# Performance work log

Measured on AMD Instinct MI355X. Metric: run time of the kernel, lower is better.

The kernel has to match this reference:

```python
import jax, jax.numpy as jnp
import numpy as np

B, N, H, D, FE = 4, 1024, 64, 64, 16  # batch, nodes, hidden_in, out_dim, edge_feat


def setup_inputs() -> dict:
    key = jax.random.key(0)
    k0, k1, k2, k3 = jax.random.split(key, 4)
    h0 = jax.random.normal(k0, (B, N, H), dtype=jnp.float32)
    e = jax.random.normal(k1, (B, N, N, FE), dtype=jnp.float32)
    # fc: Linear(H -> D, bias=False), xavier-normal-ish scale
    w_fc = jax.random.normal(k2, (D, H), dtype=jnp.float32) * (2.0 / np.sqrt(H + D))
    # attn_fc: Linear(2*D + FE -> 1, bias=False), stored as a flat vector
    w_attn = jax.random.normal(k3, (2 * D + FE,), dtype=jnp.float32) * (2.0 / np.sqrt(2 * D + FE + 1))
    return {"h0": h0, "e": e, "w_fc": w_fc, "w_attn": w_attn}


def reference(h0, e, w_fc, w_attn):
    # z = fc(h0): [B, N, D]
    z = jnp.einsum('bnh,dh->bnd', h0, w_fc)
    d = z.shape[-1]
    # attn_fc on concat(z1, z2, m): z1[i*N+j] = z[j], z2[i*N+j] = z[i], m[i*N+j] = e[i, j]
    a1, a2, a3 = w_attn[:d], w_attn[d:2 * d], w_attn[2 * d:]
    sj = jnp.einsum('bnd,d->bn', z, a1)            # score part from z1 (source j)
    si = jnp.einsum('bnd,d->bn', z, a2)            # score part from z2 (target i)
    se = jnp.einsum('bijf,f->bij', e, a3)          # edge score part
    # scores s[b, i, j], then leaky_relu (slope 0.01 as in torch default)
    s = jax.nn.leaky_relu(si[:, :, None] + sj[:, None, :] + se)
    # softmax over the flattened N*N pair axis (dim=1 of [B, N*N, 1] in torch)
    b = s.shape[0]
    alpha = jax.nn.softmax(s.reshape(b, -1), axis=1).reshape(s.shape)  # [B, N, N]
    # h_t[b, i] = sum_j alpha[b, i, j] * z_expanded[b, i, j], where z_expanded[b, i, j] = z[b, i]
    h_t = jnp.sum(alpha, axis=2)[:, :, None] * z
    return h_t
```

## Files before the change

kernel.cpp:

```cpp
#include <hip/hip_runtime.h>
#include <hip/hip_bf16.h>

#define NTOK   1024
#define NROWS  4096
#define HD     64

__global__ __launch_bounds__(256) void k1_fc(
    const float* __restrict__ h0, const float* __restrict__ w_fc,
    const float* __restrict__ w_attn,
    float* __restrict__ z, float* __restrict__ si, float* __restrict__ sj)
{
    __shared__ float wfs[HD * 65];
    __shared__ float h0s[16 * HD];

    const int tid = threadIdx.x;
    for (int k = tid; k < HD * HD; k += 256) {
        int d = k >> 6, h = k & 63;
        wfs[d * 65 + h] = w_fc[k];
    }
    const int row0 = blockIdx.x * 16;
    for (int k = tid; k < 16 * HD; k += 256)
        h0s[k] = h0[row0 * HD + k];
    __syncthreads();

    const int lane = tid & 63, wave = tid >> 6;
    const float a1 = w_attn[lane];
    const float a2 = w_attn[HD + lane];

    for (int rr = wave; rr < 16; rr += 4) {
        float acc = 0.f;
        #pragma unroll
        for (int h = 0; h < HD; ++h)
            acc = fmaf(h0s[rr * HD + h], wfs[lane * 65 + h], acc);
        const int row = row0 + rr;
        z[row * HD + lane] = acc;

        float v1 = acc * a1, v2 = acc * a2;
        #pragma unroll
        for (int off = 32; off; off >>= 1) {
            v1 += __shfl_xor(v1, off);
            v2 += __shfl_xor(v2, off);
        }
        if (lane == 0) { sj[row] = v1; si[row] = v2; }
    }
}

__global__ __launch_bounds__(256) void k2_row(
    const float* __restrict__ e, const float* __restrict__ w_attn,
    const float* __restrict__ si, const float* __restrict__ sj,
    float* __restrict__ Mrow, float* __restrict__ Rrow)
{
    const int row = blockIdx.x;
    const int b   = row >> 10;
    const int tid = threadIdx.x;

    const float4* a3v = (const float4*)(w_attn + 2 * HD);
    const float4  a3q = a3v[tid & 3];

    const float   si_r = si[row];
    const float4* ev   = (const float4*)(e + (size_t)row * (NTOK * 16));
    const float*  sjb  = sj + b * NTOK;

    float sv[16];
    #pragma unroll
    for (int it = 0; it < 16; ++it) {
        const int c = it * 256 + tid;
        const float4 ec = ev[c];
        float p = ec.x * a3q.x + ec.y * a3q.y + ec.z * a3q.z + ec.w * a3q.w;
        p += __shfl_xor(p, 1);
        p += __shfl_xor(p, 2);
        const int j = it * 64 + (tid >> 2);
        float s = si_r + sjb[j] + p;
        s = (s > 0.f) ? s : 0.01f * s;
        sv[it] = s;
    }

    float m = sv[0];
    #pragma unroll
    for (int it = 1; it < 16; ++it) m = fmaxf(m, sv[it]);
    float r = 0.f;
    #pragma unroll
    for (int it = 0; it < 16; ++it) r += __expf(sv[it] - m);

    #pragma unroll
    for (int off = 1; off < 64; off <<= 1) {
        float om  = __shfl_xor(m, off);
        float orr = __shfl_xor(r, off);
        float nm  = fmaxf(m, om);
        r = r * __expf(m - nm) + orr * __expf(om - nm);
        m = nm;
    }

    __shared__ float sm[4], sr[4];
    if ((tid & 63) == 0) { sm[tid >> 6] = m; sr[tid >> 6] = r; }
    __syncthreads();
    if (tid == 0) {
        float M = sm[0], R = sr[0];
        #pragma unroll
        for (int w = 1; w < 4; ++w) {
            float om = sm[w], orr = sr[w];
            float nm = fmaxf(M, om);
            R = R * __expf(M - nm) + orr * __expf(om - nm);
            M = nm;
        }
        Mrow[row] = M;
        Rrow[row] = R * 0.25f;
    }
}

__global__ __launch_bounds__(1024) void k3_batch(
    const float* __restrict__ Mrow, const float* __restrict__ Rrow,
    float* __restrict__ mz)
{
    const int b = blockIdx.x;
    const int i = threadIdx.x;
    const float Mi = Mrow[b * NTOK + i];
    const float Ri = Rrow[b * NTOK + i];

    __shared__ float red[16];
    __shared__ float bc;

    float m = Mi;
    #pragma unroll
    for (int off = 32; off; off >>= 1) m = fmaxf(m, __shfl_xor(m, off));
    if ((i & 63) == 0) red[i >> 6] = m;
    __syncthreads();
    if (i == 0) {
        float mm = red[0];
        #pragma unroll
        for (int w = 1; w < 16; ++w) mm = fmaxf(mm, red[w]);
        bc = mm;
    }
    __syncthreads();
    const float mb = bc;

    float ssum = Ri * __expf(Mi - mb);
    #pragma unroll
    for (int off = 32; off; off >>= 1) ssum += __shfl_xor(ssum, off);
    __syncthreads();
    if ((i & 63) == 0) red[i >> 6] = ssum;
    __syncthreads();
    if (i == 0) {
        float Z = 0.f;
        #pragma unroll
        for (int w = 0; w < 16; ++w) Z += red[w];
        mz[b * 2]     = mb;
        mz[b * 2 + 1] = Z;
    }
}

__global__ __launch_bounds__(256) void k4_out(
    const float* __restrict__ z, const float* __restrict__ Mrow,
    const float* __restrict__ Rrow, const float* __restrict__ mz,
    float* __restrict__ out)
{
    const int idx = blockIdx.x * 256 + threadIdx.x;
    const int row = idx >> 4;
    const int b   = row >> 10;
    const float scale = Rrow[row] * __expf(Mrow[row] - mz[b * 2]) / mz[b * 2 + 1];
    const float4 zv = ((const float4*)z)[idx];
    float4 o;
    o.x = zv.x * scale; o.y = zv.y * scale;
    o.z = zv.z * scale; o.w = zv.w * scale;
    ((float4*)out)[idx] = o;
}

extern "C" void kernel_launch(void* const* d_in, const int* in_sizes, int n_in,
                              void* d_out, int out_size, void* d_ws, size_t ws_size,
                              hipStream_t stream)
{
    const float* h0     = (const float*)d_in[0];
    const float* e      = (const float*)d_in[1];
    const float* w_fc   = (const float*)d_in[2];
    const float* w_attn = (const float*)d_in[3];
    float* out = (float*)d_out;

    float* ws   = (float*)d_ws;
    float* z    = ws;
    float* si   = z  + NROWS * HD;
    float* sj   = si + NROWS;
    float* Mrow = sj + NROWS;
    float* Rrow = Mrow + NROWS;
    float* mz   = Rrow + NROWS;

    k1_fc   <<<256,   256,  0, stream>>>(h0, w_fc, w_attn, z, si, sj);
    k2_row  <<<NROWS, 256,  0, stream>>>(e, w_attn, si, sj, Mrow, Rrow);
    k3_batch<<<4,     1024, 0, stream>>>(Mrow, Rrow, mz);
    k4_out  <<<256,   256,  0, stream>>>(z, Mrow, Rrow, mz, out);
}
```

Before: 373.8 us.

## Drop softmax max-stabilization and fold batch normalizer into atomics

Removes the running-max tracking from the row softmax, so each row just sums exp(score) directly. The per-batch normalizer is accumulated with atomicAdd in the row kernel, which eliminates the separate batch-reduction kernel and its launch. The normalizer is zeroed at the start of the fc kernel. This trims exp and shuffle work plus one launch, but the unstabilized exponent can overflow if scores grow large, and float atomics make the sum order nondeterministic.

```diff
diff --git a/kernel.cpp b/kernel.cpp
--- a/kernel.cpp
+++ b/kernel.cpp
@@ -8,12 +8,15 @@
 __global__ __launch_bounds__(256) void k1_fc(
     const float* __restrict__ h0, const float* __restrict__ w_fc,
     const float* __restrict__ w_attn,
-    float* __restrict__ z, float* __restrict__ si, float* __restrict__ sj)
+    float* __restrict__ z, float* __restrict__ si, float* __restrict__ sj,
+    float* __restrict__ Zb)
 {
     __shared__ float wfs[HD * 65];
     __shared__ float h0s[16 * HD];
 
     const int tid = threadIdx.x;
+    if (blockIdx.x == 0 && tid < 4) Zb[tid] = 0.f;
+
     for (int k = tid; k < HD * HD; k += 256) {
         int d = k >> 6, h = k & 63;
         wfs[d * 65 + h] = w_fc[k];
@@ -48,7 +51,7 @@
 __global__ __launch_bounds__(256) void k2_row(
     const float* __restrict__ e, const float* __restrict__ w_attn,
     const float* __restrict__ si, const float* __restrict__ sj,
-    float* __restrict__ Mrow, float* __restrict__ Rrow)
+    float* __restrict__ Rrow, float* __restrict__ Zb)
 {
     const int row = blockIdx.x;
     const int b   = row >> 10;
@@ -61,7 +64,7 @@
     const float4* ev   = (const float4*)(e + (size_t)row * (NTOK * 16));
     const float*  sjb  = sj + b * NTOK;
 
-    float sv[16];
+    float r = 0.f;
     #pragma unroll
     for (int it = 0; it < 16; ++it) {
         const int c = it * 256 + tid;
@@ -72,92 +75,31 @@
         const int j = it * 64 + (tid >> 2);
         float s = si_r + sjb[j] + p;
         s = (s > 0.f) ? s : 0.01f * s;
-        sv[it] = s;
+        r += __expf(s);
     }
 
-    float m = sv[0];
     #pragma unroll
-    for (int it = 1; it < 16; ++it) m = fmaxf(m, sv[it]);
-    float r = 0.f;
-    #pragma unroll
-    for (int it = 0; it < 16; ++it) r += __expf(sv[it] - m);
+    for (int off = 1; off < 64; off <<= 1)
+        r += __shfl_xor(r, off);
 
-    #pragma unroll
-    for (int off = 1; off < 64; off <<= 1) {
-        float om  = __shfl_xor(m, off);
-        float orr = __shfl_xor(r, off);
-        float nm  = fmaxf(m, om);
-        r = r * __expf(m - nm) + orr * __expf(om - nm);
-        m = nm;
-    }
-
-    __shared__ float sm[4], sr[4];
-    if ((tid & 63) == 0) { sm[tid >> 6] = m; sr[tid >> 6] = r; }
+    __shared__ float sr[4];
+    if ((tid & 63) == 0) sr[tid >> 6] = r;
     __syncthreads();
     if (tid == 0) {
-        float M = sm[0], R = sr[0];
-        #pragma unroll
-        for (int w = 1; w < 4; ++w) {
-            float om = sm[w], orr = sr[w];
-            float nm = fmaxf(M, om);
-            R = R * __expf(M - nm) + orr * __expf(om - nm);
-            M = nm;
-        }
-        Mrow[row] = M;
-        Rrow[row] = R * 0.25f;
-    }
-}
-
-__global__ __launch_bounds__(1024) void k3_batch(
-    const float* __restrict__ Mrow, const float* __restrict__ Rrow,
-    float* __restrict__ mz)
-{
-    const int b = blockIdx.x;
-    const int i = threadIdx.x;
-    const float Mi = Mrow[b * NTOK + i];
-    const float Ri = Rrow[b * NTOK + i];
-
-    __shared__ float red[16];
-    __shared__ float bc;
-
-    float m = Mi;
-    #pragma unroll
-    for (int off = 32; off; off >>= 1) m = fmaxf(m, __shfl_xor(m, off));
-    if ((i & 63) == 0) red[i >> 6] = m;
-    __syncthreads();
-    if (i == 0) {
-        float mm = red[0];
-        #pragma unroll
-        for (int w = 1; w < 16; ++w) mm = fmaxf(mm, red[w]);
-        bc = mm;
-    }
-    __syncthreads();
-    const float mb = bc;
-
-    float ssum = Ri * __expf(Mi - mb);
-    #pragma unroll
-    for (int off = 32; off; off >>= 1) ssum += __shfl_xor(ssum, off);
-    __syncthreads();
-    if ((i & 63) == 0) red[i >> 6] = ssum;
-    __syncthreads();
-    if (i == 0) {
-        float Z = 0.f;
-        #pragma unroll
-        for (int w = 0; w < 16; ++w) Z += red[w];
-        mz[b * 2]     = mb;
-        mz[b * 2 + 1] = Z;
+        float R = (sr[0] + sr[1] + sr[2] + sr[3]) * 0.25f;
+        Rrow[row] = R;
+        atomicAdd(&Zb[b], R);
     }
 }
 
 __global__ __launch_bounds__(256) void k4_out(
-    const float* __restrict__ z, const float* __restrict__ Mrow,
-    const float* __restrict__ Rrow, const float* __restrict__ mz,
-    float* __restrict__ out)
+    const float* __restrict__ z, const float* __restrict__ Rrow,
+    const float* __restrict__ Zb, float* __restrict__ out)
 {
     const int idx = blockIdx.x * 256 + threadIdx.x;
     const int row = idx >> 4;
     const int b   = row >> 10;
-    const float scale = Rrow[row] * __expf(Mrow[row] - mz[b * 2]) / mz[b * 2 + 1];
+    const float scale = Rrow[row] / Zb[b];
     const float4 zv = ((const float4*)z)[idx];
     float4 o;
     o.x = zv.x * scale; o.y = zv.y * scale;
@@ -179,12 +121,10 @@
     float* z    = ws;
     float* si   = z  + NROWS * HD;
     float* sj   = si + NROWS;
-    float* Mrow = sj + NROWS;
-    float* Rrow = Mrow + NROWS;
-    float* mz   = Rrow + NROWS;
+    float* Rrow = sj + NROWS;
+    float* Zb   = Rrow + NROWS;
 
-    k1_fc   <<<256,   256,  0, stream>>>(h0, w_fc, w_attn, z, si, sj);
-    k2_row  <<<NROWS, 256,  0, stream>>>(e, w_attn, si, sj, Mrow, Rrow);
-    k3_batch<<<4,     1024, 0, stream>>>(Mrow, Rrow, mz);
-    k4_out  <<<256,   256,  0, stream>>>(z, Mrow, Rrow, mz, out);
+    k1_fc  <<<256,   256, 0, stream>>>(h0, w_fc, w_attn, z, si, sj, Zb);
+    k2_row <<<NROWS, 256, 0, stream>>>(e, w_attn, si, sj, Rrow, Zb);
+    k4_out <<<256,   256, 0, stream>>>(z, Rrow, Zb, out);
 }
```

Result: no change. 371.3 us (-0.7%).
